# Performance work log

Measured on AMD Instinct MI355X. Metric: run time of the kernel, lower is better.

Reference implementation:

```python
import jax, jax.numpy as jnp
import numpy as np

B = 1048576  # batch of homography systems
PATCH = 128.0  # canonical patch size, typical for deep-homography nets


def setup_inputs() -> dict:
    key = jax.random.key(0)
    k1, k2 = jax.random.split(key)
    base = jnp.array([[0.0, 0.0], [PATCH, 0.0], [PATCH, PATCH], [0.0, PATCH]], dtype=jnp.float32)
    # jittered patch corners -> well-conditioned, nonsingular DLT systems
    corners_A = base[None, :, :] + 4.0 * jax.random.normal(k1, (B, 4, 2), dtype=jnp.float32)
    delta = 8.0 * jax.random.normal(k2, (B, 4, 2), dtype=jnp.float32)
    return {"corners_A": corners_A, "delta": delta}


def reference(corners_A, delta):
    # corners_A, delta: [B, 4, 2]
    corners_B = corners_A + delta
    u, v = corners_A[..., 0], corners_A[..., 1]    # [B, 4]
    up, vp = corners_B[..., 0], corners_B[..., 1]  # [B, 4]
    z = jnp.zeros_like(u)
    o = jnp.ones_like(u)
    # even rows (2i):   [0, 0, 0, -u, -v, -1,  vp*u,  vp*v],  b = -vp
    # odd rows  (2i+1): [u, v, 1,  0,  0,  0, -up*u, -up*v],  b =  up
    rows_even = jnp.stack([z, z, z, -u, -v, -o, vp * u, vp * v], axis=-1)  # [B, 4, 8]
    rows_odd = jnp.stack([u, v, o, z, z, z, -up * u, -up * v], axis=-1)    # [B, 4, 8]
    Bsz = corners_A.shape[0]
    A = jnp.stack([rows_even, rows_odd], axis=2).reshape(Bsz, 8, 8)  # interleave even/odd rows
    b = jnp.stack([-vp, up], axis=2).reshape(Bsz, 8, 1)
    # square 8x8 system: lstsq solution == linear solve for nonsingular A
    hhat = jnp.linalg.solve(A, b)[..., 0]  # [B, 8]
    H = jnp.concatenate([hhat, jnp.ones((Bsz, 1), dtype=hhat.dtype)], axis=-1).reshape(Bsz, 3, 3)
    return H
```

## Files before the change

kernel.cpp:

```cpp
#include <hip/hip_runtime.h>

#define THREADS 256

__global__ __launch_bounds__(THREADS) void dlt_kernel(
    const float4* __restrict__ cA,
    const float4* __restrict__ dl,
    float* __restrict__ out,
    int B)
{
    __shared__ float lds[THREADS * 9];
    const int tid = threadIdx.x;
    const int b = blockIdx.x * THREADS + tid;

    float h[9];
    #pragma unroll
    for (int k = 0; k < 9; ++k) h[k] = 0.0f;

    if (b < B) {
        const float4 c0 = cA[2 * b + 0];
        const float4 c1 = cA[2 * b + 1];
        const float4 e0 = dl[2 * b + 0];
        const float4 e1 = dl[2 * b + 1];

        const float u1 = c0.x, v1 = c0.y, u2 = c0.z, v2 = c0.w;
        const float u3 = c1.x, v3 = c1.y, u4 = c1.z, v4 = c1.w;
        const float p1 = u1 + e0.x, q1 = v1 + e0.y;
        const float p2 = u2 + e0.z, q2 = v2 + e0.w;
        const float p3 = u3 + e1.x, q3 = v3 + e1.y;
        const float p4 = u4 + e1.z, q4 = v4 + e1.w;

        #define DET3(ax,ay,bx,by,cx,cy) \
            (((bx) - (ax)) * ((cy) - (ay)) - ((cx) - (ax)) * ((by) - (ay)))

        const float D1a = DET3(u4, v4, u2, v2, u3, v3);
        const float D2a = DET3(u1, v1, u4, v4, u3, v3);
        const float D3a = DET3(u1, v1, u2, v2, u4, v4);
        const float D1b = DET3(p4, q4, p2, q2, p3, q3);
        const float D2b = DET3(p1, q1, p4, q4, p3, q3);
        const float D3b = DET3(p1, q1, p2, q2, p4, q4);

        const float k1 = D1b * (D2a * D3a);
        const float k2 = D2b * (D3a * D1a);
        const float k3 = D3b * (D1a * D2a);

        const float g1x = v2 - v3, g1y = u3 - u2, g1z = u2 * v3 - u3 * v2;
        const float g2x = v3 - v1, g2y = u1 - u3, g2z = u3 * v1 - u1 * v3;
        const float g3x = v1 - v2, g3y = u2 - u1, g3z = u1 * v2 - u2 * v1;

        const float w1 = k1 * p1, w2 = k2 * p2, w3 = k3 * p3;
        const float x1 = k1 * q1, x2 = k2 * q2, x3 = k3 * q3;

        const float H00 = w1 * g1x + w2 * g2x + w3 * g3x;
        const float H01 = w1 * g1y + w2 * g2y + w3 * g3y;
        const float H02 = w1 * g1z + w2 * g2z + w3 * g3z;
        const float H10 = x1 * g1x + x2 * g2x + x3 * g3x;
        const float H11 = x1 * g1y + x2 * g2y + x3 * g3y;
        const float H12 = x1 * g1z + x2 * g2z + x3 * g3z;
        const float H20 = k1 * g1x + k2 * g2x + k3 * g3x;
        const float H21 = k1 * g1y + k2 * g2y + k3 * g3y;
        const float H22 = k1 * g1z + k2 * g2z + k3 * g3z;

        const float r = 1.0f / H22;
        h[0] = H00 * r; h[1] = H01 * r; h[2] = H02 * r;
        h[3] = H10 * r; h[4] = H11 * r; h[5] = H12 * r;
        h[6] = H20 * r; h[7] = H21 * r; h[8] = 1.0f;
    }

    #pragma unroll
    for (int k = 0; k < 9; ++k) lds[tid * 9 + k] = h[k];
    __syncthreads();

    const long long base = (long long)blockIdx.x * (THREADS * 9);
    const long long total = (long long)B * 9;
    #pragma unroll
    for (int k = 0; k < 9; ++k) {
        const int i = k * THREADS + tid;
        const long long gi = base + i;
        if (gi < total) out[gi] = lds[i];
    }
}

extern "C" void kernel_launch(void* const* d_in, const int* in_sizes, int n_in,
                              void* d_out, int out_size, void* d_ws, size_t ws_size,
                              hipStream_t stream) {
    const int B = in_sizes[0] / 8;
    const float4* cA = (const float4*)d_in[0];
    const float4* dl = (const float4*)d_in[1];
    float* out = (float*)d_out;
    const int grid = (B + THREADS - 1) / THREADS;
    dlt_kernel<<<grid, THREADS, 0, stream>>>(cA, dl, out, B);
}
```

Before: 21.05 us.

## Use per-wave LDS staging with vectorized nontemporal stores and two systems per thread

Each wave now stages its results in its own LDS segment, so the block-wide __syncthreads is no longer needed. The output is written back as float4 nontemporal stores instead of scalar stores. Each thread solves two systems and loads its inputs with nontemporal loads, which halves the grid and raises memory-level parallelism. A scalar fallback path handles partial tails, at the cost of more registers per thread and fewer blocks.

```diff
diff --git a/kernel.cpp b/kernel.cpp
--- a/kernel.cpp
+++ b/kernel.cpp
@@ -1,82 +1,121 @@
 #include <hip/hip_runtime.h>
 
 #define THREADS 256
+#define WAVES 4
+#define SPT 2
+#define SEG 64
+#define SYS_PER_BLOCK (THREADS * SPT)
+#define SEG_FLOATS (SEG * 9)
+#define SEG_VEC4 (SEG_FLOATS / 4)
+#define BLOCK_VEC4 (SYS_PER_BLOCK * 9 / 4)
+
+typedef float vfloat4 __attribute__((ext_vector_type(4)));
+
+__device__ __forceinline__ void solve_h(const vfloat4 c0, const vfloat4 c1,
+                                        const vfloat4 e0, const vfloat4 e1,
+                                        float h[9])
+{
+    const float u1 = c0.x, v1 = c0.y, u2 = c0.z, v2 = c0.w;
+    const float u3 = c1.x, v3 = c1.y, u4 = c1.z, v4 = c1.w;
+    const float p1 = u1 + e0.x, q1 = v1 + e0.y;
+    const float p2 = u2 + e0.z, q2 = v2 + e0.w;
+    const float p3 = u3 + e1.x, q3 = v3 + e1.y;
+    const float p4 = u4 + e1.z, q4 = v4 + e1.w;
+
+    #define DET3(ax,ay,bx,by,cx,cy) \
+        (((bx) - (ax)) * ((cy) - (ay)) - ((cx) - (ax)) * ((by) - (ay)))
+
+    const float D1a = DET3(u4, v4, u2, v2, u3, v3);
+    const float D2a = DET3(u1, v1, u4, v4, u3, v3);
+    const float D3a = DET3(u1, v1, u2, v2, u4, v4);
+    const float D1b = DET3(p4, q4, p2, q2, p3, q3);
+    const float D2b = DET3(p1, q1, p4, q4, p3, q3);
+    const float D3b = DET3(p1, q1, p2, q2, p4, q4);
+
+    const float k1 = D1b * (D2a * D3a);
+    const float k2 = D2b * (D3a * D1a);
+    const float k3 = D3b * (D1a * D2a);
+
+    const float g1x = v2 - v3, g1y = u3 - u2, g1z = u2 * v3 - u3 * v2;
+    const float g2x = v3 - v1, g2y = u1 - u3, g2z = u3 * v1 - u1 * v3;
+    const float g3x = v1 - v2, g3y = u2 - u1, g3z = u1 * v2 - u2 * v1;
+
+    const float w1 = k1 * p1, w2 = k2 * p2, w3 = k3 * p3;
+    const float x1 = k1 * q1, x2 = k2 * q2, x3 = k3 * q3;
+
+    const float H22 = k1 * g1z + k2 * g2z + k3 * g3z;
+    const float r = 1.0f / H22;
+
+    h[0] = (w1 * g1x + w2 * g2x + w3 * g3x) * r;
+    h[1] = (w1 * g1y + w2 * g2y + w3 * g3y) * r;
+    h[2] = (w1 * g1z + w2 * g2z + w3 * g3z) * r;
+    h[3] = (x1 * g1x + x2 * g2x + x3 * g3x) * r;
+    h[4] = (x1 * g1y + x2 * g2y + x3 * g3y) * r;
+    h[5] = (x1 * g1z + x2 * g2z + x3 * g3z) * r;
+    h[6] = (k1 * g1x + k2 * g2x + k3 * g3x) * r;
+    h[7] = (k1 * g1y + k2 * g2y + k3 * g3y) * r;
+    h[8] = 1.0f;
+}
 
 __global__ __launch_bounds__(THREADS) void dlt_kernel(
-    const float4* __restrict__ cA,
-    const float4* __restrict__ dl,
+    const vfloat4* __restrict__ cA,
+    const vfloat4* __restrict__ dl,
+    vfloat4* __restrict__ out4,
     float* __restrict__ out,
     int B)
 {
-    __shared__ float lds[THREADS * 9];
-    const int tid = threadIdx.x;
-    const int b = blockIdx.x * THREADS + tid;
+    __shared__ float lds[WAVES][SPT][SEG_FLOATS];
+    const int tid  = threadIdx.x;
+    const int lane = tid & 63;
+    const int wave = tid >> 6;
+    const int blockSysBase = blockIdx.x * SYS_PER_BLOCK;
+    const int waveSysBase = blockSysBase + wave * (SPT * SEG);
 
-    float h[9];
-    #pragma unroll
-    for (int k = 0; k < 9; ++k) h[k] = 0.0f;
+    if (waveSysBase + SPT * SEG <= B) {
+        const int g0 = waveSysBase + lane;
+        const int g1 = g0 + SEG;
 
-    if (b < B) {
-        const float4 c0 = cA[2 * b + 0];
-        const float4 c1 = cA[2 * b + 1];
-        const float4 e0 = dl[2 * b + 0];
-        const float4 e1 = dl[2 * b + 1];
+        const vfloat4 a00 = __builtin_nontemporal_load(&cA[2 * g0 + 0]);
+        const vfloat4 a01 = __builtin_nontemporal_load(&cA[2 * g0 + 1]);
+        const vfloat4 d00 = __builtin_nontemporal_load(&dl[2 * g0 + 0]);
+        const vfloat4 d01 = __builtin_nontemporal_load(&dl[2 * g0 + 1]);
+        const vfloat4 a10 = __builtin_nontemporal_load(&cA[2 * g1 + 0]);
+        const vfloat4 a11 = __builtin_nontemporal_load(&cA[2 * g1 + 1]);
+        const vfloat4 d10 = __builtin_nontemporal_load(&dl[2 * g1 + 0]);
+        const vfloat4 d11 = __builtin_nontemporal_load(&dl[2 * g1 + 1]);
 
-        const float u1 = c0.x, v1 = c0.y, u2 = c0.z, v2 = c0.w;
-        const float u3 = c1.x, v3 = c1.y, u4 = c1.z, v4 = c1.w;
-        const float p1 = u1 + e0.x, q1 = v1 + e0.y;
-        const float p2 = u2 + e0.z, q2 = v2 + e0.w;
-        const float p3 = u3 + e1.x, q3 = v3 + e1.y;
-        const float p4 = u4 + e1.z, q4 = v4 + e1.w;
+        #pragma unroll
+        for (int s = 0; s < SPT; ++s) {
+            float h[9];
+            if (s == 0) solve_h(a00, a01, d00, d01, h);
+            else        solve_h(a10, a11, d10, d11, h);
 
-        #define DET3(ax,ay,bx,by,cx,cy) \
-            (((bx) - (ax)) * ((cy) - (ay)) - ((cx) - (ax)) * ((by) - (ay)))
+            float* buf = &lds[wave][s][0];
+            #pragma unroll
+            for (int k = 0; k < 9; ++k) buf[lane * 9 + k] = h[k];
 
-        const float D1a = DET3(u4, v4, u2, v2, u3, v3);
-        const float D2a = DET3(u1, v1, u4, v4, u3, v3);
-        const float D3a = DET3(u1, v1, u2, v2, u4, v4);
-        const float D1b = DET3(p4, q4, p2, q2, p3, q3);
-        const float D2b = DET3(p1, q1, p4, q4, p3, q3);
-        const float D3b = DET3(p1, q1, p2, q2, p4, q4);
-
-        const float k1 = D1b * (D2a * D3a);
-        const float k2 = D2b * (D3a * D1a);
-        const float k3 = D3b * (D1a * D2a);
-
-        const float g1x = v2 - v3, g1y = u3 - u2, g1z = u2 * v3 - u3 * v2;
-        const float g2x = v3 - v1, g2y = u1 - u3, g2z = u3 * v1 - u1 * v3;
-        const float g3x = v1 - v2, g3y = u2 - u1, g3z = u1 * v2 - u2 * v1;
-
-        const float w1 = k1 * p1, w2 = k2 * p2, w3 = k3 * p3;
-        const float x1 = k1 * q1, x2 = k2 * q2, x3 = k3 * q3;
-
-        const float H00 = w1 * g1x + w2 * g2x + w3 * g3x;
-        const float H01 = w1 * g1y + w2 * g2y + w3 * g3y;
-        const float H02 = w1 * g1z + w2 * g2z + w3 * g3z;
-        const float H10 = x1 * g1x + x2 * g2x + x3 * g3x;
-        const float H11 = x1 * g1y + x2 * g2y + x3 * g3y;
-        const float H12 = x1 * g1z + x2 * g2z + x3 * g3z;
-        const float H20 = k1 * g1x + k2 * g2x + k3 * g3x;
-        const float H21 = k1 * g1y + k2 * g2y + k3 * g3y;
-        const float H22 = k1 * g1z + k2 * g2z + k3 * g3z;
-
-        const float r = 1.0f / H22;
-        h[0] = H00 * r; h[1] = H01 * r; h[2] = H02 * r;
-        h[3] = H10 * r; h[4] = H11 * r; h[5] = H12 * r;
-        h[6] = H20 * r; h[7] = H21 * r; h[8] = 1.0f;
-    }
-
-    #pragma unroll
-    for (int k = 0; k < 9; ++k) lds[tid * 9 + k] = h[k];
-    __syncthreads();
-
-    const long long base = (long long)blockIdx.x * (THREADS * 9);
-    const long long total = (long long)B * 9;
-    #pragma unroll
-    for (int k = 0; k < 9; ++k) {
-        const int i = k * THREADS + tid;
-        const long long gi = base + i;
-        if (gi < total) out[gi] = lds[i];
+            const vfloat4* buf4 = (const vfloat4*)buf;
+            const int segBase4 = (waveSysBase + s * SEG) * 9 / 4;
+            __builtin_nontemporal_store(buf4[lane],      &out4[segBase4 + lane]);
+            __builtin_nontemporal_store(buf4[lane + 64], &out4[segBase4 + lane + 64]);
+            if (lane < SEG_VEC4 - 128)
+                __builtin_nontemporal_store(buf4[lane + 128], &out4[segBase4 + lane + 128]);
+        }
+    } else {
+        #pragma unroll
+        for (int s = 0; s < SPT; ++s) {
+            const int b = waveSysBase + s * SEG + lane;
+            if (b < B) {
+                const vfloat4 c0 = cA[2 * b + 0];
+                const vfloat4 c1 = cA[2 * b + 1];
+                const vfloat4 e0 = dl[2 * b + 0];
+                const vfloat4 e1 = dl[2 * b + 1];
+                float h[9];
+                solve_h(c0, c1, e0, e1, h);
+                #pragma unroll
+                for (int k = 0; k < 9; ++k) out[b * 9 + k] = h[k];
+            }
+        }
     }
 }
 
@@ -84,9 +123,10 @@
                               void* d_out, int out_size, void* d_ws, size_t ws_size,
                               hipStream_t stream) {
     const int B = in_sizes[0] / 8;
-    const float4* cA = (const float4*)d_in[0];
-    const float4* dl = (const float4*)d_in[1];
+    const vfloat4* cA = (const vfloat4*)d_in[0];
+    const vfloat4* dl = (const vfloat4*)d_in[1];
+    vfloat4* out4 = (vfloat4*)d_out;
     float* out = (float*)d_out;
-    const int grid = (B + THREADS - 1) / THREADS;
-    dlt_kernel<<<grid, THREADS, 0, stream>>>(cA, dl, out, B);
+    const int grid = (B + SYS_PER_BLOCK - 1) / SYS_PER_BLOCK;
+    dlt_kernel<<<grid, THREADS, 0, stream>>>(cA, dl, out4, out, B);
 }
```

After: 23.98 us. +13.9%, slower.
